# Optimization experiments

Measured on AMD Instinct MI355X. Metric: run time of the kernel, lower is better.

The kernel has to match this reference:

```python
import jax, jax.numpy as jnp
import numpy as np

B, T, DIM, H, DH, DT = 2, 2048, 1024, 16, 64, 32
Q_TEMP, K_TEMP = 1.0, 1.0
EPS = float(np.finfo(np.float32).eps)  # torch RMSNorm default eps for fp32
INV_SQRT_DH = 1.0 / np.sqrt(DH)


def _get_time(length, head_time_delta, time_angles, with_time_delta):
    # [T,1,1] positions, optionally offset per head -> [T,H,1]
    pos = jnp.arange(length, dtype=jnp.float32)[:, None, None]
    if with_time_delta:
        pos = pos + head_time_delta[None, :, None]          # [T,H,1]
    else:
        pos = jnp.broadcast_to(pos, (length, H, 1))          # [T,H,1]
    ang = pos * time_angles                                  # [T,H,Dt]
    c, s = jnp.cos(ang), jnp.sin(ang)
    return jnp.concatenate([c + s, c - s], axis=-1) * INV_SQRT_DH  # [T,H,2Dt]


def setup_inputs() -> dict:
    key = jax.random.key(0)
    ks = jax.random.split(key, 6)
    sc = 0.02
    states = jax.random.normal(ks[0], (B, T, DIM), jnp.float32)
    attention_mask = jnp.ones((B, T), jnp.int32)
    ln_w = jnp.ones((DIM,), jnp.float32)
    time_angles = 10000.0 ** (-1.0 / jnp.arange(1, DT + 1, dtype=jnp.float32))
    head_time_delta = jax.random.uniform(ks[1], (H,), jnp.float32)
    Wq = jax.random.normal(ks[2], (H * DH, DIM), jnp.float32) * sc
    q_bias = jnp.zeros((H * DH,), jnp.float32)
    Wk = jax.random.normal(ks[3], (H * DH, DIM), jnp.float32) * sc
    bk = jnp.zeros((H * DH,), jnp.float32)
    Wv = jax.random.normal(ks[4], (H * DH, DIM), jnp.float32) * sc
    bv = jnp.zeros((H * DH,), jnp.float32)
    Wo = jax.random.normal(ks[5], (DIM, H * DH), jnp.float32) * sc
    bo = jnp.zeros((DIM,), jnp.float32)
    return dict(states=states, attention_mask=attention_mask, ln_w=ln_w,
                time_angles=time_angles, head_time_delta=head_time_delta,
                Wq=Wq, q_bias=q_bias, Wk=Wk, bk=bk, Wv=Wv, bv=bv, Wo=Wo, bo=bo)


def reference(states, attention_mask, ln_w, time_angles, head_time_delta,
              Wq, q_bias, Wk, bk, Wv, bv, Wo, bo):
    # RMSNorm
    x = states * jax.lax.rsqrt(jnp.mean(states * states, axis=-1, keepdims=True) + EPS) * ln_w
    m = attention_mask.astype(x.dtype)[:, :, None, None]   # [B,T,1,1]

    # Q path -> q_attentioned [B,T,T,H]
    q = (x @ Wq.T - jnp.exp(q_bias)).reshape(B, T, H, DH)
    q_sm = jax.nn.softmax(q / Q_TEMP * m, axis=-1)
    t_q = _get_time(T, head_time_delta, time_angles, True)   # [T,H,2Dt]
    t_k = _get_time(T, head_time_delta, time_angles, False)  # [T,H,2Dt]
    q_timed = jnp.sum(q_sm, axis=-1, keepdims=True) * t_q    # [B,T,H,2Dt]
    q_att = jnp.einsum('bthd,lhd->btlh', q_timed, t_k)       # [B,T,T,H]

    # KV path
    k = (x @ Wk.T + bk).reshape(B, T, H, DH)
    k_sm = jax.nn.softmax(k / K_TEMP * m, axis=-1)
    v = (x @ Wv.T + bv).reshape(B, T, H, DH)
    kv = k_sm * v                                            # [B,T,H,Dh]

    loading = jnp.einsum('btlh,blhd->bthd', q_att, kv)       # [B,T,H,Dh]
    return loading.reshape(B, T, DIM) @ Wo.T + bo
```

## Files before the change

kernel.cpp:

```cpp
#include <hip/hip_runtime.h>
#include <math.h>

#define T_ 2048
#define H_ 16

typedef __attribute__((ext_vector_type(8))) short bfx8;
typedef __attribute__((ext_vector_type(4))) float f32x4;

__device__ __forceinline__ short f2bf(float f) {
  union { float f; unsigned u; } x; x.f = f;
  unsigned r = (x.u + 0x7FFFu + ((x.u >> 16) & 1u)) >> 16;
  return (short)r;
}
__device__ __forceinline__ float bf2f(short s) {
  union { unsigned u; float f; } x;
  x.u = ((unsigned)(unsigned short)s) << 16;
  return x.f;
}

#define GLD_LDS(g, l) \
  __builtin_amdgcn_global_load_lds( \
      (const __attribute__((address_space(1))) void*)(g), \
      (__attribute__((address_space(3))) void*)(l), 16, 0, 0)

__global__ __launch_bounds__(256) void prep_kernel(
    const float* __restrict__ Wk, const float* __restrict__ Wv,
    const float* __restrict__ Wo, const float* __restrict__ angles,
    const float* __restrict__ states, const float* __restrict__ ln_w,
    short* __restrict__ Wkb, short* __restrict__ Wvb, short* __restrict__ Wob,
    short* __restrict__ xb, short* __restrict__ Cb, short* __restrict__ tkT,
    float* __restrict__ MtH) {
  const int blk = blockIdx.x;
  if (blk < 3072) {
    const int i = blk * 256 + threadIdx.x;
    const int which = i >> 18;
    const int idx = i & 262143;
    const float* s = (which == 0) ? Wk : (which == 1) ? Wv : Wo;
    short* d = (which == 0) ? Wkb : (which == 1) ? Wvb : Wob;
    const float4 v = ((const float4*)s)[idx];
    short4 r;
    r.x = f2bf(v.x); r.y = f2bf(v.y); r.z = f2bf(v.z); r.w = f2bf(v.w);
    ((short4*)d)[idx] = r;
  } else if (blk < 7168) {
    const int row = blk - 3072;
    const int tid = threadIdx.x;
    const float4 v = ((const float4*)(states + (size_t)row * 1024))[tid];
    float ss = v.x * v.x + v.y * v.y + v.z * v.z + v.w * v.w;
#pragma unroll
    for (int off = 32; off >= 1; off >>= 1) ss += __shfl_xor(ss, off);
    __shared__ float red[4];
    if ((tid & 63) == 0) red[tid >> 6] = ss;
    __syncthreads();
    const float tot = red[0] + red[1] + red[2] + red[3];
    const float scale = rsqrtf(tot * (1.0f / 1024.0f) + 1.1920928955078125e-07f);
    const float4 w = ((const float4*)ln_w)[tid];
    short4 o;
    o.x = f2bf(v.x * scale * w.x);
    o.y = f2bf(v.y * scale * w.y);
    o.z = f2bf(v.z * scale * w.z);
    o.w = f2bf(v.w * scale * w.w);
    ((short4*)(xb + (size_t)row * 1024))[tid] = o;
  } else if (blk < 7424) {
    const int gid = (blk - 7168) * 256 + threadIdx.x;
    const int j = gid & 31;
    const int t = gid >> 5;
    float s, c;
    sincosf((float)t * angles[j], &s, &c);
    Cb[(size_t)t * 64 + j] = f2bf(0.125f * c);
    Cb[(size_t)t * 64 + 32 + j] = f2bf(0.125f * s);
  } else if (blk < 7456) {
    const int gid = (blk - 7424) * 256 + threadIdx.x;
    const int tc = gid & 255;
    const int j = gid >> 8;
    const float th = angles[j];
    short lo[8], hi[8];
#pragma unroll
    for (int r = 0; r < 8; ++r) {
      float s, c;
      sincosf((float)(tc * 8 + r) * th, &s, &c);
      lo[r] = f2bf((c + s) * 0.125f);
      hi[r] = f2bf((c - s) * 0.125f);
    }
    short* base = tkT + (size_t)j * 2048 + tc * 8;
    *(short4*)(base) = *(short4*)&lo[0];
    *(short4*)(base + 4) = *(short4*)&lo[4];
    short* base2 = tkT + (size_t)(32 + j) * 2048 + tc * 8;
    *(short4*)(base2) = *(short4*)&hi[0];
    *(short4*)(base2 + 4) = *(short4*)&hi[4];
  } else {
    const int gid = (blk - 7456) * 256 + threadIdx.x;
    ((float4*)MtH)[gid] = make_float4(0.f, 0.f, 0.f, 0.f);
  }
}

__global__ __launch_bounds__(512, 4) void kvgemm_kernel(
    const short* __restrict__ xb, const short* __restrict__ Wkb,
    const short* __restrict__ Wvb, const float* __restrict__ bk,
    const float* __restrict__ bv, const int* __restrict__ mask,
    const short* __restrict__ tkT, float* __restrict__ Mt) {
  __shared__ short smem[16384];
  __shared__ short Vs[128][64];
  short(*As)[64] = (short(*)[64])smem;
  short(*Bk)[64] = (short(*)[64])(smem + 8192);
  short(*Bv)[64] = (short(*)[64])(smem + 12288);
  short(*kvS)[132] = (short(*)[132])smem;

  const int row0 = blockIdx.x * 128;
  const int h = blockIdx.y;
  const int t = threadIdx.x;
  const int lane = t & 63;
  const int wv = t >> 6;
  const bool isV = wv >= 4;
  const int wrow = (wv & 3) * 32;
  const int lrow = lane & 15;

  const int srow8 = t >> 3;
  const int kslotS = (t & 7) ^ (srow8 & 7);
  const short* gaS = xb + (size_t)(row0 + srow8) * 1024 + kslotS * 8;
  const short* gkS = Wkb + (size_t)(h * 64 + srow8) * 1024 + kslotS * 8;
  const short* gvS = Wvb + (size_t)(h * 64 + srow8) * 1024 + kslotS * 8;
  short* laS = &As[srow8][(t & 7) * 8];
  short* lkS = &Bk[srow8][(t & 7) * 8];
  short* lvS = &Bv[srow8][(t & 7) * 8];

  f32x4 acc[2][4] = {};
  for (int k0 = 0; k0 < 1024; k0 += 64) {
    GLD_LDS(gaS + k0, laS);
    GLD_LDS(gaS + 64 * 1024 + k0, laS + 4096);
    GLD_LDS(gkS + k0, lkS);
    GLD_LDS(gvS + k0, lvS);
    __syncthreads();
#pragma unroll
    for (int kk = 0; kk < 2; ++kk) {
      const int pcol = ((kk * 4 + (lane >> 4)) ^ (lrow & 7)) * 8;
      bfx8 af[2], bf_[4];
#pragma unroll
      for (int i = 0; i < 2; ++i)
        af[i] = *(const bfx8*)&As[wrow + i * 16 + lrow][pcol];
      const short(*Bs)[64] = isV ? Bv : Bk;
#pragma unroll
      for (int j = 0; j < 4; ++j)
        bf_[j] = *(const bfx8*)&Bs[j * 16 + lrow][pcol];
#pragma unroll
      for (int i = 0; i < 2; ++i)
#pragma unroll
        for (int j = 0; j < 4; ++j)
          acc[i][j] = __builtin_amdgcn_mfma_f32_16x16x32_bf16(af[i], bf_[j], acc[i][j], 0, 0, 0);
    }
    __syncthreads();
  }
  const int rq = (lane >> 4) * 4;
  if (isV) {
#pragma unroll
    for (int j = 0; j < 4; ++j) {
      const float bb = bv[h * 64 + j * 16 + lrow];
#pragma unroll
      for (int i = 0; i < 2; ++i)
#pragma unroll
        for (int rr = 0; rr < 4; ++rr)
          Vs[wrow + rq + i * 16 + rr][j * 16 + lrow] = f2bf(acc[i][j][rr] + bb);
    }
  }
  __syncthreads();
  if (!isV) {
    float bkc[4];
#pragma unroll
    for (int j = 0; j < 4; ++j) bkc[j] = bk[h * 64 + j * 16 + lrow];
    const int rowg0 = row0 + wrow + rq;
#pragma unroll
    for (int i = 0; i < 2; ++i) {
#pragma unroll
      for (int rr = 0; rr < 4; ++rr) {
        const float m = (float)mask[rowg0 + i * 16 + rr];
        float kf[4];
#pragma unroll
        for (int j = 0; j < 4; ++j) kf[j] = (acc[i][j][rr] + bkc[j]) * m;
        float mx = fmaxf(fmaxf(kf[0], kf[1]), fmaxf(kf[2], kf[3]));
#pragma unroll
        for (int off = 8; off >= 1; off >>= 1) mx = fmaxf(mx, __shfl_xor(mx, off));
        float s = 0.0f;
#pragma unroll
        for (int j = 0; j < 4; ++j) { kf[j] = expf(kf[j] - mx); s += kf[j]; }
#pragma unroll
        for (int off = 8; off >= 1; off >>= 1) s += __shfl_xor(s, off);
        const float inv = 1.0f / s;
#pragma unroll
        for (int j = 0; j < 4; ++j)
          acc[i][j][rr] = kf[j] * inv *
                          bf2f(Vs[wrow + rq + i * 16 + rr][j * 16 + lrow]);
      }
    }
#pragma unroll
    for (int j = 0; j < 4; ++j) {
      const int d = j * 16 + lrow;
#pragma unroll
      for (int i = 0; i < 2; ++i) {
        short4 o;
        o.x = f2bf(acc[i][j][0]); o.y = f2bf(acc[i][j][1]);
        o.z = f2bf(acc[i][j][2]); o.w = f2bf(acc[i][j][3]);
        *(short4*)&kvS[d][wrow + rq + i * 16] = o;
      }
    }
  }
  __syncthreads();
  if (wv < 4) {
    const int bb = row0 >> 11;
    const int tb = row0 & 2047;
    const short* tkb = tkT + (size_t)(wv * 16 + lrow) * 2048 + tb;
    const int kg = (lane >> 4) * 8;
    f32x4 macc[4] = {};
#pragma unroll
    for (int kc = 0; kc < 4; ++kc) {
      const bfx8 af = *(const bfx8*)(tkb + kc * 32 + kg);
#pragma unroll
      for (int j = 0; j < 4; ++j) {
        const bfx8 bf_ = *(const bfx8*)&kvS[j * 16 + lrow][kc * 32 + kg];
        macc[j] = __builtin_amdgcn_mfma_f32_16x16x32_bf16(af, bf_, macc[j], 0, 0, 0);
      }
    }
    float* Mb = Mt + (size_t)(bb * 16 + h) * 4096;
#pragma unroll
    for (int j = 0; j < 4; ++j) {
      const int d = j * 16 + lrow;
#pragma unroll
      for (int rr = 0; rr < 4; ++rr) {
        const int e = wv * 16 + rq + rr;
        atomicAdd(&Mb[(size_t)e * 64 + d], macc[j][rr]);
      }
    }
  }
}

__global__ __launch_bounds__(256) void foldhgemm_kernel(
    const short* __restrict__ Wob, const float* __restrict__ Mt,
    const float* __restrict__ angles, const float* __restrict__ delta,
    float* __restrict__ H) {
  const int bid = blockIdx.x;
  const int t = threadIdx.x;
  const int lane = t & 63;
  const int w = t >> 6;
  const int lrow = lane & 15;
  const int kg = (lane >> 4) * 8;
  const int h2 = bid & 7;
  const int ot = (bid >> 3) & 15;
  const int b = bid >> 7;
  const int orow = ot * 64 + w * 16 + lrow;
  float p[2][2], q[2][2];
#pragma unroll
  for (int hh = 0; hh < 2; ++hh) {
    const float dl = delta[h2 * 2 + hh];
#pragma unroll
    for (int aa = 0; aa < 2; ++aa) {
      float s, c;
      sincosf(dl * angles[aa * 16 + lrow], &s, &c);
      p[hh][aa] = c + s;
      q[hh][aa] = c - s;
    }
  }
  f32x4 acc[4] = {};
#pragma unroll
  for (int ks = 0; ks < 4; ++ks) {
    const int hh = ks >> 1;
    const int h = h2 * 2 + hh;
    const int d0 = (ks & 1) * 32 + kg;
    const float* Mthb = Mt + (size_t)(b * 16 + h) * 4096;
    const bfx8 af = *(const bfx8*)(Wob + (size_t)orow * 1024 + h * 64 + d0);
    float m0a[8], m1a[8], m0b[8], m1b[8];
    *(float4*)&m0a[0] = *(const float4*)(Mthb + lrow * 64 + d0);
    *(float4*)&m0a[4] = *(const float4*)(Mthb + lrow * 64 + d0 + 4);
    *(float4*)&m1a[0] = *(const float4*)(Mthb + (32 + lrow) * 64 + d0);
    *(float4*)&m1a[4] = *(const float4*)(Mthb + (32 + lrow) * 64 + d0 + 4);
    *(float4*)&m0b[0] = *(const float4*)(Mthb + (16 + lrow) * 64 + d0);
    *(float4*)&m0b[4] = *(const float4*)(Mthb + (16 + lrow) * 64 + d0 + 4);
    *(float4*)&m1b[0] = *(const float4*)(Mthb + (48 + lrow) * 64 + d0);
    *(float4*)&m1b[4] = *(const float4*)(Mthb + (48 + lrow) * 64 + d0 + 4);
    bfx8 bf0, bf1, bf2, bf3;
#pragma unroll
    for (int e = 0; e < 8; ++e) {
      bf0[e] = f2bf(p[hh][0] * m0a[e] + q[hh][0] * m1a[e]);
      bf1[e] = f2bf(p[hh][1] * m0b[e] + q[hh][1] * m1b[e]);
      bf2[e] = f2bf(q[hh][0] * m0a[e] - p[hh][0] * m1a[e]);
      bf3[e] = f2bf(q[hh][1] * m0b[e] - p[hh][1] * m1b[e]);
    }
    acc[0] = __builtin_amdgcn_mfma_f32_16x16x32_bf16(af, bf0, acc[0], 0, 0, 0);
    acc[1] = __builtin_amdgcn_mfma_f32_16x16x32_bf16(af, bf1, acc[1], 0, 0, 0);
    acc[2] = __builtin_amdgcn_mfma_f32_16x16x32_bf16(af, bf2, acc[2], 0, 0, 0);
    acc[3] = __builtin_amdgcn_mfma_f32_16x16x32_bf16(af, bf3, acc[3], 0, 0, 0);
  }
  float* Hb = H + (size_t)b * 65536;
  const int rq = (lane >> 4) * 4;
#pragma unroll
  for (int j = 0; j < 4; ++j) {
    const int kap = j * 16 + lrow;
#pragma unroll
    for (int rr = 0; rr < 4; ++rr) {
      const int o = ot * 64 + w * 16 + rq + rr;
      atomicAdd(&Hb[(size_t)o * 64 + kap], acc[j][rr]);
    }
  }
}

__global__ __launch_bounds__(256) void ofinal_kernel(
    const short* __restrict__ Cb, const float* __restrict__ H,
    const float* __restrict__ bo, float* __restrict__ out) {
  const int col0 = blockIdx.x * 128;
  const int row0 = blockIdx.y * 128;
  const int b = blockIdx.z;
  float* C = out + (size_t)b * 2097152;
  const float* Hb = H + (size_t)b * 65536;
  const int t = threadIdx.x;
  const int lane = t & 63;
  const int wv = t >> 6;
  const int wm = (wv & 1) * 64, wn = (wv >> 1) * 64;
  const int lrow = lane & 15;
  const int kg = (lane >> 4) * 8;
  f32x4 acc[4][4] = {};
#pragma unroll
  for (int k0 = 0; k0 < 64; k0 += 32) {
    bfx8 af[4], bf_[4];
#pragma unroll
    for (int i = 0; i < 4; ++i)
      af[i] = *(const bfx8*)(Cb + (size_t)(row0 + wm + i * 16 + lrow) * 64 + k0 + kg);
#pragma unroll
    for (int j = 0; j < 4; ++j) {
      const float* hp = Hb + (size_t)(col0 + wn + j * 16 + lrow) * 64 + k0 + kg;
      const float4 h0 = *(const float4*)hp;
      const float4 h1 = *(const float4*)(hp + 4);
      bfx8 bb;
      bb[0] = f2bf(h0.x); bb[1] = f2bf(h0.y); bb[2] = f2bf(h0.z); bb[3] = f2bf(h0.w);
      bb[4] = f2bf(h1.x); bb[5] = f2bf(h1.y); bb[6] = f2bf(h1.z); bb[7] = f2bf(h1.w);
      bf_[j] = bb;
    }
#pragma unroll
    for (int i = 0; i < 4; ++i)
#pragma unroll
      for (int j = 0; j < 4; ++j)
        acc[i][j] = __builtin_amdgcn_mfma_f32_16x16x32_bf16(af[i], bf_[j], acc[i][j], 0, 0, 0);
  }
  const int rq = (lane >> 4) * 4;
#pragma unroll
  for (int j = 0; j < 4; ++j) {
    const int c = col0 + wn + j * 16 + lrow;
    const float bb = bo[c];
#pragma unroll
    for (int i = 0; i < 4; ++i) {
      const int r = row0 + wm + i * 16 + rq;
#pragma unroll
      for (int rr = 0; rr < 4; ++rr)
        C[(size_t)(r + rr) * 1024 + c] = acc[i][j][rr] + bb;
    }
  }
}

extern "C" void kernel_launch(void* const* d_in, const int* in_sizes, int n_in,
                              void* d_out, int out_size, void* d_ws, size_t ws_size,
                              hipStream_t stream) {
  (void)in_sizes; (void)n_in; (void)out_size; (void)ws_size;
  const float* states = (const float*)d_in[0];
  const int* mask = (const int*)d_in[1];
  const float* ln_w = (const float*)d_in[2];
  const float* angles = (const float*)d_in[3];
  const float* delta = (const float*)d_in[4];
  const float* Wk = (const float*)d_in[7];
  const float* bk = (const float*)d_in[8];
  const float* Wv = (const float*)d_in[9];
  const float* bv = (const float*)d_in[10];
  const float* Wo = (const float*)d_in[11];
  const float* bo = (const float*)d_in[12];
  float* out = (float*)d_out;

  char* W = (char*)d_ws;
  short* xb  = (short*)(W);
  short* Wkb = (short*)(W + (8u << 20));
  short* Wvb = (short*)(W + (10u << 20));
  short* Wob = (short*)(W + (12u << 20));
  short* Cb  = (short*)(W + (14u << 20));
  short* tkT = (short*)(W + (14u << 20) + (256u << 10));
  float* Mt  = (float*)(W + (15u << 20));
  float* H   = (float*)(W + (15u << 20) + (512u << 10));

  prep_kernel<<<7712, 256, 0, stream>>>(Wk, Wv, Wo, angles, states, ln_w,
                                        Wkb, Wvb, Wob, xb, Cb, tkT, Mt);
  kvgemm_kernel<<<dim3(32, 16), 512, 0, stream>>>(xb, Wkb, Wvb, bk, bv, mask,
                                                  tkT, Mt);
  foldhgemm_kernel<<<256, 256, 0, stream>>>(Wob, Mt, angles, delta, H);
  ofinal_kernel<<<dim3(8, 16, 2), 256, 0, stream>>>(Cb, H, bo, out);
}
```

Before: 145.0 us.

## Double kvgemm block to 1024 threads with 16-row wave tiles and aliased LDS

The K/V projection kernel now runs 16 waves per block instead of 8. Each wave computes a 16-row by 64-column tile instead of 32 rows, and each thread issues two global-to-LDS loads per k-step instead of four. The separate V staging buffer is dropped: V and the kv transpose now reuse the dead GEMM tiles in shared memory, which shrinks LDS per block. This spreads the work over more waves with fewer registers each, but the launch bound of (1024, 8) may push the compiler into very tight register limits and spills.

```diff
diff --git a/kernel.cpp b/kernel.cpp
--- a/kernel.cpp
+++ b/kernel.cpp
@@ -93,59 +93,52 @@
   }
 }
 
-__global__ __launch_bounds__(512, 4) void kvgemm_kernel(
+__global__ __launch_bounds__(1024, 8) void kvgemm_kernel(
     const short* __restrict__ xb, const short* __restrict__ Wkb,
     const short* __restrict__ Wvb, const float* __restrict__ bk,
     const float* __restrict__ bv, const int* __restrict__ mask,
     const short* __restrict__ tkT, float* __restrict__ Mt) {
-  __shared__ short smem[16384];
-  __shared__ short Vs[128][64];
+  __shared__ short smem[16640];
   short(*As)[64] = (short(*)[64])smem;
   short(*Bk)[64] = (short(*)[64])(smem + 8192);
   short(*Bv)[64] = (short(*)[64])(smem + 12288);
-  short(*kvS)[132] = (short(*)[132])smem;
+  short(*Vs)[64] = (short(*)[64])smem;
+  short(*kvS)[132] = (short(*)[132])(smem + 8192);
 
   const int row0 = blockIdx.x * 128;
   const int h = blockIdx.y;
   const int t = threadIdx.x;
   const int lane = t & 63;
   const int wv = t >> 6;
-  const bool isV = wv >= 4;
-  const int wrow = (wv & 3) * 32;
+  const bool isV = wv >= 8;
+  const int wrow = (wv & 7) * 16;
   const int lrow = lane & 15;
 
   const int srow8 = t >> 3;
   const int kslotS = (t & 7) ^ (srow8 & 7);
   const short* gaS = xb + (size_t)(row0 + srow8) * 1024 + kslotS * 8;
-  const short* gkS = Wkb + (size_t)(h * 64 + srow8) * 1024 + kslotS * 8;
-  const short* gvS = Wvb + (size_t)(h * 64 + srow8) * 1024 + kslotS * 8;
+  const short* gbS = isV ? Wvb + (size_t)(h * 64 + srow8 - 64) * 1024 + kslotS * 8
+                         : Wkb + (size_t)(h * 64 + srow8) * 1024 + kslotS * 8;
   short* laS = &As[srow8][(t & 7) * 8];
-  short* lkS = &Bk[srow8][(t & 7) * 8];
-  short* lvS = &Bv[srow8][(t & 7) * 8];
-
-  f32x4 acc[2][4] = {};
+  short* lbS = isV ? &Bv[srow8 - 64][(t & 7) * 8] : &Bk[srow8][(t & 7) * 8];
+
+  f32x4 acc[4] = {};
   for (int k0 = 0; k0 < 1024; k0 += 64) {
     GLD_LDS(gaS + k0, laS);
-    GLD_LDS(gaS + 64 * 1024 + k0, laS + 4096);
-    GLD_LDS(gkS + k0, lkS);
-    GLD_LDS(gvS + k0, lvS);
+    GLD_LDS(gbS + k0, lbS);
     __syncthreads();
 #pragma unroll
     for (int kk = 0; kk < 2; ++kk) {
       const int pcol = ((kk * 4 + (lane >> 4)) ^ (lrow & 7)) * 8;
-      bfx8 af[2], bf_[4];
-#pragma unroll
-      for (int i = 0; i < 2; ++i)
-        af[i] = *(const bfx8*)&As[wrow + i * 16 + lrow][pcol];
+      const bfx8 af = *(const bfx8*)&As[wrow + lrow][pcol];
       const short(*Bs)[64] = isV ? Bv : Bk;
+      bfx8 bf_[4];
 #pragma unroll
       for (int j = 0; j < 4; ++j)
         bf_[j] = *(const bfx8*)&Bs[j * 16 + lrow][pcol];
 #pragma unroll
-      for (int i = 0; i < 2; ++i)
-#pragma unroll
-        for (int j = 0; j < 4; ++j)
-          acc[i][j] = __builtin_amdgcn_mfma_f32_16x16x32_bf16(af[i], bf_[j], acc[i][j], 0, 0, 0);
+      for (int j = 0; j < 4; ++j)
+        acc[j] = __builtin_amdgcn_mfma_f32_16x16x32_bf16(af, bf_[j], acc[j], 0, 0, 0);
     }
     __syncthreads();
   }
@@ -155,10 +148,8 @@
     for (int j = 0; j < 4; ++j) {
       const float bb = bv[h * 64 + j * 16 + lrow];
 #pragma unroll
-      for (int i = 0; i < 2; ++i)
-#pragma unroll
-        for (int rr = 0; rr < 4; ++rr)
-          Vs[wrow + rq + i * 16 + rr][j * 16 + lrow] = f2bf(acc[i][j][rr] + bb);
+      for (int rr = 0; rr < 4; ++rr)
+        Vs[wrow + rq + rr][j * 16 + lrow] = f2bf(acc[j][rr] + bb);
     }
   }
   __syncthreads();
@@ -168,38 +159,31 @@
     for (int j = 0; j < 4; ++j) bkc[j] = bk[h * 64 + j * 16 + lrow];
     const int rowg0 = row0 + wrow + rq;
 #pragma unroll
-    for (int i = 0; i < 2; ++i) {
-#pragma unroll
-      for (int rr = 0; rr < 4; ++rr) {
-        const float m = (float)mask[rowg0 + i * 16 + rr];
-        float kf[4];
-#pragma unroll
-        for (int j = 0; j < 4; ++j) kf[j] = (acc[i][j][rr] + bkc[j]) * m;
-        float mx = fmaxf(fmaxf(kf[0], kf[1]), fmaxf(kf[2], kf[3]));
-#pragma unroll
-        for (int off = 8; off >= 1; off >>= 1) mx = fmaxf(mx, __shfl_xor(mx, off));
-        float s = 0.0f;
-#pragma unroll
-        for (int j = 0; j < 4; ++j) { kf[j] = expf(kf[j] - mx); s += kf[j]; }
-#pragma unroll
-        for (int off = 8; off >= 1; off >>= 1) s += __shfl_xor(s, off);
-        const float inv = 1.0f / s;
-#pragma unroll
-        for (int j = 0; j < 4; ++j)
-          acc[i][j][rr] = kf[j] * inv *
-                          bf2f(Vs[wrow + rq + i * 16 + rr][j * 16 + lrow]);
-      }
+    for (int rr = 0; rr < 4; ++rr) {
+      const float m = (float)mask[rowg0 + rr];
+      float kf[4];
+#pragma unroll
+      for (int j = 0; j < 4; ++j) kf[j] = (acc[j][rr] + bkc[j]) * m;
+      float mx = fmaxf(fmaxf(kf[0], kf[1]), fmaxf(kf[2], kf[3]));
+#pragma unroll
+      for (int off = 8; off >= 1; off >>= 1) mx = fmaxf(mx, __shfl_xor(mx, off));
+      float s = 0.0f;
+#pragma unroll
+      for (int j = 0; j < 4; ++j) { kf[j] = expf(kf[j] - mx); s += kf[j]; }
+#pragma unroll
+      for (int off = 8; off >= 1; off >>= 1) s += __shfl_xor(s, off);
+      const float inv = 1.0f / s;
+#pragma unroll
+      for (int j = 0; j < 4; ++j)
+        acc[j][rr] = kf[j] * inv * bf2f(Vs[wrow + rq + rr][j * 16 + lrow]);
     }
 #pragma unroll
     for (int j = 0; j < 4; ++j) {
       const int d = j * 16 + lrow;
-#pragma unroll
-      for (int i = 0; i < 2; ++i) {
-        short4 o;
-        o.x = f2bf(acc[i][j][0]); o.y = f2bf(acc[i][j][1]);
-        o.z = f2bf(acc[i][j][2]); o.w = f2bf(acc[i][j][3]);
-        *(short4*)&kvS[d][wrow + rq + i * 16] = o;
-      }
+      short4 o;
+      o.x = f2bf(acc[j][0]); o.y = f2bf(acc[j][1]);
+      o.z = f2bf(acc[j][2]); o.w = f2bf(acc[j][3]);
+      *(short4*)&kvS[d][wrow + rq] = o;
     }
   }
   __syncthreads();
@@ -381,8 +365,8 @@
 
   prep_kernel<<<7712, 256, 0, stream>>>(Wk, Wv, Wo, angles, states, ln_w,
                                         Wkb, Wvb, Wob, xb, Cb, tkT, Mt);
-  kvgemm_kernel<<<dim3(32, 16), 512, 0, stream>>>(xb, Wkb, Wvb, bk, bv, mask,
-                                                  tkT, Mt);
+  kvgemm_kernel<<<dim3(32, 16), 1024, 0, stream>>>(xb, Wkb, Wvb, bk, bv, mask,
+                                                   tkT, Mt);
   foldhgemm_kernel<<<256, 256, 0, stream>>>(Wob, Mt, angles, delta, H);
   ofinal_kernel<<<dim3(8, 16, 2), 256, 0, stream>>>(Cb, H, bo, out);
 }
```

Measured after the change: 143.7 us. Within noise of the previous version (-0.9%).
